# Kernel tuning notes

Measured on AMD Instinct MI355X. Metric: run time of the kernel, lower is better.

Reference implementation:

```python
import jax, jax.numpy as jnp
import numpy as np

S, H, NUM_TAG, D_LEN, MAX_LEN = 256, 1024, 20, 10, 1000


def setup_inputs() -> dict:
    key = jax.random.key(0)
    ks = jax.random.split(key, 6)
    sc = lambda d: 1.0 / np.sqrt(d)
    return {
        "hidden": jax.random.normal(ks[0], (S, H), jnp.float32),
        "target": jax.random.randint(ks[1], (S,), 0, NUM_TAG),
        "attn_w1": jax.random.normal(ks[2], (H, H), jnp.float32) * sc(H),
        "attn_b1": jnp.zeros((H,), jnp.float32),
        "attn_w2": jax.random.normal(ks[3], (H, 1), jnp.float32) * sc(H),
        "attn_b2": jnp.zeros((1,), jnp.float32),
        "len_emb": jax.random.normal(ks[4], (MAX_LEN, D_LEN), jnp.float32),
        "fc_w": jax.random.normal(ks[5], (3 * H + D_LEN, NUM_TAG), jnp.float32) * sc(3 * H + D_LEN),
        "fc_b": jnp.zeros((NUM_TAG,), jnp.float32),
    }


def reference(hidden, target, attn_w1, attn_b1, attn_w2, attn_b2, len_emb, fc_w, fc_b):
    S_, H_ = hidden.shape
    # attention scores [S]
    a = (jnp.tanh(hidden @ attn_w1 + attn_b1) @ attn_w2 + attn_b2)[:, 0]
    # prefix sums for contiguous-window softmax pooling
    e = jnp.exp(a - jnp.max(a))                                   # [S]
    Zc = jnp.concatenate([jnp.zeros((1,), e.dtype), jnp.cumsum(e)])                      # [S+1]
    Pc = jnp.concatenate([jnp.zeros((1, H_), e.dtype), jnp.cumsum(e[:, None] * hidden, axis=0)])  # [S+1,H]
    ii, jj = jnp.triu_indices(S_, k=1)                            # all spans i<j, loop order
    span = (Pc[jj + 1] - Pc[ii]) / (Zc[jj + 1] - Zc[ii])[:, None]  # softmax-weighted pooling
    lemb = len_emb[jj - ii + 1]                                   # segment length embedding (no grad in torch)
    feats = jnp.concatenate([span, hidden[ii], hidden[jj], lemb], axis=-1)  # [P, 3H+10]
    logits = feats @ fc_w + fc_b                                  # [P, num_tag]
    # is_span labels via run ids
    change = jnp.concatenate([jnp.array([True]), target[1:] != target[:-1]])
    run_id = jnp.cumsum(change.astype(jnp.int32))
    start = change
    end = jnp.concatenate([target[:-1] != target[1:], jnp.array([True])])
    labels = jnp.where((run_id[ii] == run_id[jj]) & start[ii] & end[jj], target[jj], 0)
    logp = jax.nn.log_softmax(logits, axis=-1)
    loss = -jnp.mean(jnp.take_along_axis(logp, labels[:, None].astype(jnp.int32), axis=1))
    return logits, loss.reshape(1)
```

## Files before the change

### kernel.cpp

```cpp
#include <hip/hip_runtime.h>
#include <math.h>

#define S 256
#define H 1024
#define NTAG 20
#define NPAIR 32640

#define WS_T     0
#define WS_HP    2097152
#define WS_A     2220032
#define WS_ZC    2220544
#define WS_HW0   2220804
#define WS_HW1   2225924
#define WS_HW2   2231044
#define WS_PW    2236164
#define WS_LW    2241304
#define WS_LOSSP 2246444
#define WS_RUN   2246572
#define WS_START 2246828
#define WS_END   2247084

__global__ __launch_bounds__(256) void kG(const float* __restrict__ hidden,
                                          const float* __restrict__ w1,
                                          const float* __restrict__ fcw,
                                          float* __restrict__ ws) {
    const int tid = threadIdx.x;
    const int b = blockIdx.x;
    __shared__ __align__(16) float shbuf[128 * 20];

    if (b < 512) {
        const int cg = b & 3, rg = (b >> 2) & 15, kc = b >> 6;
        float (*shH)[20] = (float(*)[20])shbuf;
        const int kk = tid & 127;
        const int r0 = (tid >> 7) * 8;
        #pragma unroll
        for (int e = 0; e < 8; e++)
            shH[kk][r0 + e] = hidden[(rg * 16 + r0 + e) * H + kc * 128 + kk];
        __syncthreads();

        float acc[16];
        #pragma unroll
        for (int r = 0; r < 16; r++) acc[r] = 0.f;

        const float* wp = w1 + (size_t)(kc * 128) * H + cg * 256 + tid;
        #pragma unroll 4
        for (int k = 0; k < 128; k++) {
            const float wv = wp[k * H];
            const float4 h0 = *(const float4*)&shH[k][0];
            const float4 h1 = *(const float4*)&shH[k][4];
            const float4 h2 = *(const float4*)&shH[k][8];
            const float4 h3 = *(const float4*)&shH[k][12];
            acc[0]  = fmaf(h0.x, wv, acc[0]);  acc[1]  = fmaf(h0.y, wv, acc[1]);
            acc[2]  = fmaf(h0.z, wv, acc[2]);  acc[3]  = fmaf(h0.w, wv, acc[3]);
            acc[4]  = fmaf(h1.x, wv, acc[4]);  acc[5]  = fmaf(h1.y, wv, acc[5]);
            acc[6]  = fmaf(h1.z, wv, acc[6]);  acc[7]  = fmaf(h1.w, wv, acc[7]);
            acc[8]  = fmaf(h2.x, wv, acc[8]);  acc[9]  = fmaf(h2.y, wv, acc[9]);
            acc[10] = fmaf(h2.z, wv, acc[10]); acc[11] = fmaf(h2.w, wv, acc[11]);
            acc[12] = fmaf(h3.x, wv, acc[12]); acc[13] = fmaf(h3.y, wv, acc[13]);
            acc[14] = fmaf(h3.z, wv, acc[14]); acc[15] = fmaf(h3.w, wv, acc[15]);
        }
        float* op = ws + WS_T + kc * (S * H) + (rg * 16) * H + cg * 256 + tid;
        #pragma unroll
        for (int r = 0; r < 16; r++) op[r * H] = acc[r];
    } else {
        const int hb = b - 512;
        const int rg = hb & 15, kc = hb >> 4;
        float (*shHT)[17] = (float(*)[17])shbuf;
        {
            const int c = tid & 127, rr = tid >> 7;
            #pragma unroll
            for (int e = 0; e < 8; e++) {
                const int r = e * 2 + rr;
                shHT[c][r] = hidden[(rg * 16 + r) * H + kc * 128 + c];
            }
        }
        __syncthreads();
        if (tid < 240) {
            const int t = tid % 20, g = tid / 20;
            const int p = g >> 2, rsub = g & 3;
            const float* fw = fcw + (size_t)(p * H + kc * 128) * 20 + t;
            float a0 = 0.f, a1 = 0.f, a2 = 0.f, a3 = 0.f;
            #pragma unroll 8
            for (int k = 0; k < 128; k++) {
                const float w = fw[k * 20];
                a0 = fmaf(shHT[k][rsub * 4 + 0], w, a0);
                a1 = fmaf(shHT[k][rsub * 4 + 1], w, a1);
                a2 = fmaf(shHT[k][rsub * 4 + 2], w, a2);
                a3 = fmaf(shHT[k][rsub * 4 + 3], w, a3);
            }
            float* hp = ws + WS_HP + ((size_t)(kc * 3 + p) * 256 + rg * 16 + rsub * 4) * 20 + t;
            hp[0]  = a0; hp[20] = a1; hp[40] = a2; hp[60] = a3;
        }
    }
}

__global__ __launch_bounds__(256) void kR(const float* __restrict__ b1,
                                          const float* __restrict__ w2,
                                          float* __restrict__ ws) {
    const int b = blockIdx.x, tid = threadIdx.x;
    __shared__ float sred[256];
    float lacc = 0.f;
    #pragma unroll
    for (int q = 0; q < 4; q++) {
        const int c = q * 256 + tid;
        float sum = 0.f;
        #pragma unroll
        for (int kcz = 0; kcz < 8; kcz++)
            sum += ws[WS_T + kcz * (S * H) + b * H + c];
        lacc += tanhf(sum + b1[c]) * w2[c];
    }
    sred[tid] = lacc;
    __syncthreads();
    for (int off = 128; off > 0; off >>= 1) {
        if (tid < off) sred[tid] += sred[tid + off];
        __syncthreads();
    }
    if (tid == 0) ws[WS_A + b] = sred[0];

    if (tid < 60) {
        const int t = tid % 20, p = tid / 20;
        float s = 0.f;
        #pragma unroll
        for (int kc = 0; kc < 8; kc++)
            s += ws[WS_HP + ((size_t)(kc * 3 + p) * 256 + b) * 20 + t];
        const int base = (p == 0) ? WS_HW0 : (p == 1) ? WS_HW1 : WS_HW2;
        ws[base + b * 20 + t] = s;
    }
}

__global__ __launch_bounds__(256) void kS(const float* __restrict__ b2,
                                          const int* __restrict__ target,
                                          const float* __restrict__ lenemb,
                                          const float* __restrict__ fcw,
                                          float* __restrict__ ws) {
    const int s = threadIdx.x;
    __shared__ float shf[256], she[256];
    __shared__ int shi[256], shtg[256];
    __shared__ float shw0[5120];

    for (int item = s; item < 255 * 20; item += 256) {
        const int L = 2 + item / 20, t = item % 20;
        float v = 0.f;
        #pragma unroll
        for (int d = 0; d < 10; d++)
            v = fmaf(lenemb[L * 10 + d], fcw[(3072 + d) * 20 + t], v);
        ws[WS_LW + L * 20 + t] = v;
    }

    shtg[s] = target[s];
    const float a = ws[WS_A + s] + b2[0];
    shf[s] = a;
    __syncthreads();
    for (int off = 128; off > 0; off >>= 1) {
        if (s < off) shf[s] = fmaxf(shf[s], shf[s + off]);
        __syncthreads();
    }
    const float mx = shf[0];
    __syncthreads();
    const float ev = expf(a - mx);
    she[s] = ev;
    shf[s] = ev;
    const int chg = (s == 0) ? 1 : (shtg[s] != shtg[s - 1]);
    shi[s] = chg;
    __syncthreads();
    for (int off = 1; off < 256; off <<= 1) {
        const float fv = (s >= off) ? shf[s - off] : 0.f;
        const int   iv = (s >= off) ? shi[s - off] : 0;
        __syncthreads();
        shf[s] += fv;
        shi[s] += iv;
        __syncthreads();
    }
    ws[WS_ZC + s + 1] = shf[s];
    if (s == 0) ws[WS_ZC] = 0.f;
    ((int*)ws)[WS_RUN + s]   = shi[s];
    ((int*)ws)[WS_START + s] = chg;
    ((int*)ws)[WS_END + s]   = (s == 255) ? 1 : (shtg[s] != shtg[s + 1]);

    for (int idx = s; idx < 5120; idx += 256) shw0[idx] = ws[WS_HW0 + idx];
    __syncthreads();
    if (s < 20) {
        float pw = 0.f;
        ws[WS_PW + s] = 0.f;
        for (int s2 = 0; s2 < 256; s2++) {
            pw = fmaf(she[s2], shw0[s2 * 20 + s], pw);
            ws[WS_PW + (s2 + 1) * 20 + s] = pw;
        }
    }
}

__global__ __launch_bounds__(256) void kE(const int* __restrict__ target,
                                          const float* __restrict__ fcb,
                                          float* __restrict__ out,
                                          float* __restrict__ ws) {
    const int tid = threadIdx.x;
    const int p = blockIdx.x * 256 + tid;
    __shared__ float sred[256];
    float lossacc = 0.f;
    if (p < NPAIR) {
        int i = (int)((511.0f - sqrtf((float)(261121 - 8 * p))) * 0.5f);
        while ((i + 1) * (510 - i) <= 2 * p) ++i;
        while (i > 0 && i * (511 - i) > 2 * p) --i;
        const int j = p - i * (511 - i) / 2 + i + 1;

        const float Zci  = ws[WS_ZC + i];
        const float invz = 1.f / (ws[WS_ZC + j + 1] - Zci);
        const int L = j - i + 1;
        const int* runid = (const int*)ws + WS_RUN;
        const int* stA   = (const int*)ws + WS_START;
        const int* enA   = (const int*)ws + WS_END;
        const int lbl = (runid[i] == runid[j] && stA[i] && enA[j]) ? target[j] : 0;

        const float4* pwj4 = (const float4*)(ws + WS_PW + (j + 1) * 20);
        const float4* pwi4 = (const float4*)(ws + WS_PW + i * 20);
        const float4* h14  = (const float4*)(ws + WS_HW1 + i * 20);
        const float4* h24  = (const float4*)(ws + WS_HW2 + j * 20);
        const float4* lw4  = (const float4*)(ws + WS_LW + L * 20);
        const float4* fb4  = (const float4*)fcb;
        float4* op4 = (float4*)(out + (size_t)p * 20);

        float lg[20];
        float mx = -1e30f, chosen = 0.f;
        #pragma unroll
        for (int q = 0; q < 5; q++) {
            const float4 aj = pwj4[q], ai = pwi4[q];
            const float4 bi = h14[q],  bj = h24[q];
            const float4 cl = lw4[q],  fb = fb4[q];
            float4 r;
            r.x = (aj.x - ai.x) * invz + bi.x + bj.x + cl.x + fb.x;
            r.y = (aj.y - ai.y) * invz + bi.y + bj.y + cl.y + fb.y;
            r.z = (aj.z - ai.z) * invz + bi.z + bj.z + cl.z + fb.z;
            r.w = (aj.w - ai.w) * invz + bi.w + bj.w + cl.w + fb.w;
            op4[q] = r;
            lg[q * 4 + 0] = r.x; lg[q * 4 + 1] = r.y;
            lg[q * 4 + 2] = r.z; lg[q * 4 + 3] = r.w;
            mx = fmaxf(mx, fmaxf(fmaxf(r.x, r.y), fmaxf(r.z, r.w)));
            chosen = (q * 4 + 0 == lbl) ? r.x : chosen;
            chosen = (q * 4 + 1 == lbl) ? r.y : chosen;
            chosen = (q * 4 + 2 == lbl) ? r.z : chosen;
            chosen = (q * 4 + 3 == lbl) ? r.w : chosen;
        }
        float se = 0.f;
        #pragma unroll
        for (int t = 0; t < 20; t++) se += expf(lg[t] - mx);
        lossacc = -(chosen - mx - logf(se));
    }
    sred[tid] = lossacc;
    __syncthreads();
    for (int off = 128; off > 0; off >>= 1) {
        if (tid < off) sred[tid] += sred[tid + off];
        __syncthreads();
    }
    if (tid == 0) ws[WS_LOSSP + blockIdx.x] = sred[0];
}

__global__ __launch_bounds__(128) void kF(float* __restrict__ out,
                                          float* __restrict__ ws) {
    __shared__ float sh[128];
    const int t = threadIdx.x;
    sh[t] = ws[WS_LOSSP + t];
    __syncthreads();
    for (int off = 64; off > 0; off >>= 1) {
        if (t < off) sh[t] += sh[t + off];
        __syncthreads();
    }
    if (t == 0) out[(size_t)NPAIR * 20] = sh[0] / (float)NPAIR;
}

extern "C" void kernel_launch(void* const* d_in, const int* in_sizes, int n_in,
                              void* d_out, int out_size, void* d_ws, size_t ws_size,
                              hipStream_t stream) {
    (void)in_sizes; (void)n_in; (void)out_size; (void)ws_size;
    const float* hidden = (const float*)d_in[0];
    const int*   target = (const int*)d_in[1];
    const float* w1     = (const float*)d_in[2];
    const float* b1     = (const float*)d_in[3];
    const float* w2     = (const float*)d_in[4];
    const float* b2     = (const float*)d_in[5];
    const float* lenemb = (const float*)d_in[6];
    const float* fcw    = (const float*)d_in[7];
    const float* fcb    = (const float*)d_in[8];
    float* out = (float*)d_out;
    float* ws  = (float*)d_ws;

    kG<<<640, 256, 0, stream>>>(hidden, w1, fcw, ws);
    kR<<<256, 256, 0, stream>>>(b1, w2, ws);
    kS<<<1, 256, 0, stream>>>(b2, target, lenemb, fcw, ws);
    kE<<<128, 256, 0, stream>>>(target, fcb, out, ws);
    kF<<<1, 128, 0, stream>>>(out, ws);
}
```

Before: 44.67 us.

## Fuse final loss reduction, parallelize prefix scan, use fast math intrinsics

```diff
diff --git a/kernel.cpp b/kernel.cpp
--- a/kernel.cpp
+++ b/kernel.cpp
@@ -19,6 +19,7 @@
 #define WS_RUN   2246572
 #define WS_START 2246828
 #define WS_END   2247084
+#define WS_CTR   2247340
 
 __global__ __launch_bounds__(256) void kG(const float* __restrict__ hidden,
                                           const float* __restrict__ w1,
@@ -107,7 +108,9 @@
         #pragma unroll
         for (int kcz = 0; kcz < 8; kcz++)
             sum += ws[WS_T + kcz * (S * H) + b * H + c];
-        lacc += tanhf(sum + b1[c]) * w2[c];
+        const float x = fminf(fmaxf(sum + b1[c], -15.f), 15.f);
+        const float ex = __expf(2.f * x);
+        lacc += ((ex - 1.f) / (ex + 1.f)) * w2[c];
     }
     sred[tid] = lacc;
     __syncthreads();
@@ -136,28 +139,39 @@
     const int s = threadIdx.x;
     __shared__ float shf[256], she[256];
     __shared__ int shi[256], shtg[256];
+    __shared__ float shlen[2550];
+    __shared__ float shfct[200];
     __shared__ float shw0[5120];
-
-    for (int item = s; item < 255 * 20; item += 256) {
-        const int L = 2 + item / 20, t = item % 20;
-        float v = 0.f;
-        #pragma unroll
-        for (int d = 0; d < 10; d++)
-            v = fmaf(lenemb[L * 10 + d], fcw[(3072 + d) * 20 + t], v);
-        ws[WS_LW + L * 20 + t] = v;
-    }
+    __shared__ float shpw[5120];
+    __shared__ float soff[4][20];
+
+    if (s == 0) ((int*)ws)[WS_CTR] = 0;
+
+    for (int idx = s; idx < 2550; idx += 256) shlen[idx] = lenemb[20 + idx];
+    if (s < 200) shfct[s] = fcw[61440 + s];
+    for (int idx = s; idx < 5120; idx += 256) shw0[idx] = ws[WS_HW0 + idx];
 
     shtg[s] = target[s];
     const float a = ws[WS_A + s] + b2[0];
     shf[s] = a;
     __syncthreads();
+
+    for (int item = s; item < 5100; item += 256) {
+        const int L2i = item / 20, t = item % 20;
+        float v = 0.f;
+        #pragma unroll
+        for (int d = 0; d < 10; d++)
+            v = fmaf(shlen[L2i * 10 + d], shfct[d * 20 + t], v);
+        ws[WS_LW + (L2i + 2) * 20 + t] = v;
+    }
+
     for (int off = 128; off > 0; off >>= 1) {
         if (s < off) shf[s] = fmaxf(shf[s], shf[s + off]);
         __syncthreads();
     }
     const float mx = shf[0];
     __syncthreads();
-    const float ev = expf(a - mx);
+    const float ev = __expf(a - mx);
     she[s] = ev;
     shf[s] = ev;
     const int chg = (s == 0) ? 1 : (shtg[s] != shtg[s - 1]);
@@ -177,15 +191,25 @@
     ((int*)ws)[WS_START + s] = chg;
     ((int*)ws)[WS_END + s]   = (s == 255) ? 1 : (shtg[s] != shtg[s + 1]);
 
-    for (int idx = s; idx < 5120; idx += 256) shw0[idx] = ws[WS_HW0 + idx];
+    if (s < 80) {
+        const int t = s % 20, seg = s / 20;
+        const int base = seg * 64;
+        float pw = 0.f;
+        for (int k = 0; k < 64; k++) {
+            pw = fmaf(she[base + k], shw0[(base + k) * 20 + t], pw);
+            shpw[(base + k) * 20 + t] = pw;
+        }
+    }
     __syncthreads();
     if (s < 20) {
-        float pw = 0.f;
-        ws[WS_PW + s] = 0.f;
-        for (int s2 = 0; s2 < 256; s2++) {
-            pw = fmaf(she[s2], shw0[s2 * 20 + s], pw);
-            ws[WS_PW + (s2 + 1) * 20 + s] = pw;
-        }
+        const float T0 = shpw[63 * 20 + s], T1 = shpw[127 * 20 + s], T2 = shpw[191 * 20 + s];
+        soff[0][s] = 0.f; soff[1][s] = T0; soff[2][s] = T0 + T1; soff[3][s] = T0 + T1 + T2;
+    }
+    __syncthreads();
+    for (int item = s; item < 5140; item += 256) {
+        const int r = item / 20, t = item % 20;
+        const float v = (r == 0) ? 0.f : shpw[(r - 1) * 20 + t] + soff[(r - 1) >> 6][t];
+        ws[WS_PW + item] = v;
     }
 }
 
@@ -196,6 +220,7 @@
     const int tid = threadIdx.x;
     const int p = blockIdx.x * 256 + tid;
     __shared__ float sred[256];
+    __shared__ int sticket;
     float lossacc = 0.f;
     if (p < NPAIR) {
         int i = (int)((511.0f - sqrtf((float)(261121 - 8 * p))) * 0.5f);
@@ -242,8 +267,8 @@
         }
         float se = 0.f;
         #pragma unroll
-        for (int t = 0; t < 20; t++) se += expf(lg[t] - mx);
-        lossacc = -(chosen - mx - logf(se));
+        for (int t = 0; t < 20; t++) se += __expf(lg[t] - mx);
+        lossacc = -(chosen - mx - __logf(se));
     }
     sred[tid] = lossacc;
     __syncthreads();
@@ -251,20 +276,22 @@
         if (tid < off) sred[tid] += sred[tid + off];
         __syncthreads();
     }
-    if (tid == 0) ws[WS_LOSSP + blockIdx.x] = sred[0];
-}
-
-__global__ __launch_bounds__(128) void kF(float* __restrict__ out,
-                                          float* __restrict__ ws) {
-    __shared__ float sh[128];
-    const int t = threadIdx.x;
-    sh[t] = ws[WS_LOSSP + t];
-    __syncthreads();
-    for (int off = 64; off > 0; off >>= 1) {
-        if (t < off) sh[t] += sh[t + off];
-        __syncthreads();
-    }
-    if (t == 0) out[(size_t)NPAIR * 20] = sh[0] / (float)NPAIR;
+    if (tid == 0) {
+        ws[WS_LOSSP + blockIdx.x] = sred[0];
+        __threadfence();
+        sticket = atomicAdd((int*)ws + WS_CTR, 1);
+    }
+    __syncthreads();
+    if (sticket == 127) {
+        __threadfence();
+        sred[tid] = (tid < 128) ? ws[WS_LOSSP + tid] : 0.f;
+        __syncthreads();
+        for (int off = 64; off > 0; off >>= 1) {
+            if (tid < off) sred[tid] += sred[tid + off];
+            __syncthreads();
+        }
+        if (tid == 0) out[(size_t)NPAIR * 20] = sred[0] / (float)NPAIR;
+    }
 }
 
 extern "C" void kernel_launch(void* const* d_in, const int* in_sizes, int n_in,
@@ -287,5 +314,4 @@
     kR<<<256, 256, 0, stream>>>(b1, w2, ws);
     kS<<<1, 256, 0, stream>>>(b2, target, lenemb, fcw, ws);
     kE<<<128, 256, 0, stream>>>(target, fcb, out, ws);
-    kF<<<1, 128, 0, stream>>>(out, ws);
-}
+}
```

After: 45.45 us. About the same (+1.8%).
